# Performance work log

Measured on AMD Instinct MI355X. Metric: run time of the kernel, lower is better.

## Reference

```python
import jax, jax.numpy as jnp
import numpy as np

N_HEAD = 16


def setup_inputs() -> dict:
    key = jax.random.key(0)
    ks = jax.random.split(key, 9)
    d = 1024
    s = 0.02
    return {
        "x": jax.random.normal(ks[0], (8, 448, d), jnp.float32),
        "xa": jax.random.normal(ks[1], (8, 1500, d), jnp.float32),
        "Wq": jax.random.normal(ks[2], (d, d), jnp.float32) * s,
        "bq": jax.random.normal(ks[3], (d,), jnp.float32) * s,
        "Wk": jax.random.normal(ks[4], (d, d), jnp.float32) * s,
        "Wv": jax.random.normal(ks[5], (d, d), jnp.float32) * s,
        "bv": jax.random.normal(ks[6], (d,), jnp.float32) * s,
        "Wo": jax.random.normal(ks[7], (d, d), jnp.float32) * s,
        "bo": jax.random.normal(ks[8], (d,), jnp.float32) * s,
    }


def reference(x, xa, Wq, bq, Wk, Wv, bv, Wo, bo):
    B, T, D = x.shape
    S = xa.shape[1]
    H = N_HEAD
    Dh = D // H
    scale = Dh ** -0.25  # applied to both q and k, as in the original

    q = x @ Wq + bq            # [B,T,D]
    k = xa @ Wk                # [B,S,D] (no bias)
    v = xa @ Wv + bv           # [B,S,D]

    q = q.reshape(B, T, H, Dh) * scale
    k = k.reshape(B, S, H, Dh) * scale
    v = v.reshape(B, S, H, Dh)

    qk = jnp.einsum("bthd,bshd->bhts", q, k).astype(jnp.float32)  # pre-softmax logits
    w = jax.nn.softmax(qk, axis=-1).astype(q.dtype)
    wv = jnp.einsum("bhts,bshd->bthd", w, v).reshape(B, T, D)

    out = wv @ Wo + bo
    return out, qk
```

## Files before the change

### kernel.cpp

```cpp
#include <hip/hip_runtime.h>
#include <hip/hip_bf16.h>
#include <cstdint>
#include <cstddef>

typedef __bf16  bf16x8  __attribute__((ext_vector_type(8)));
typedef float   f32x4   __attribute__((ext_vector_type(4)));
typedef ushort  ushort8 __attribute__((ext_vector_type(8)));

#define ASYNC16(gp, lp)                                                        \
  __builtin_amdgcn_global_load_lds(                                            \
      (const __attribute__((address_space(1))) void*)(gp),                     \
      (__attribute__((address_space(3))) void*)(lp), 16, 0, 0)

__device__ __forceinline__ ushort f2bf(float f) {
  __hip_bfloat16 h = __float2bfloat16(f);
  ushort u; __builtin_memcpy(&u, &h, 2); return u;
}

#define SINF (-1e30f)

__global__ __launch_bounds__(256) void transpose_w(
    const float* __restrict__ W0, const float* __restrict__ W1,
    const float* __restrict__ W2, const float* __restrict__ W3,
    ushort* __restrict__ out) {
  __shared__ float tile[32][33];
  const float* W = blockIdx.z == 0 ? W0 : blockIdx.z == 1 ? W1
                 : blockIdx.z == 2 ? W2 : W3;
  ushort* T = out + (size_t)blockIdx.z * (1024u * 1024u);
  const int n0 = blockIdx.x * 32, k0 = blockIdx.y * 32;
  const int t = threadIdx.x;
  const int r = t >> 3, c = (t & 7) * 4;
  float4 v = *(const float4*)&W[(size_t)(k0 + r) * 1024 + n0 + c];
  tile[r][c + 0] = v.x; tile[r][c + 1] = v.y;
  tile[r][c + 2] = v.z; tile[r][c + 3] = v.w;
  __syncthreads();
  ushort4 o;
  o.x = f2bf(tile[c + 0][r]); o.y = f2bf(tile[c + 1][r]);
  o.z = f2bf(tile[c + 2][r]); o.w = f2bf(tile[c + 3][r]);
  *(ushort4*)&T[(size_t)(n0 + r) * 1024 + k0 + c] = o;
}

template <bool A_F32, bool C_F32>
__global__ __launch_bounds__(256) void gemm_bt(
    const void* __restrict__ Ap, const ushort* __restrict__ Bt,
    const float* __restrict__ bias, void* __restrict__ Cp,
    int M, float scale) {
  __shared__ ushort As[128 * 32];
  __shared__ ushort Bs[128 * 32];
  const int tid  = threadIdx.x;
  const int lane = tid & 63, w = tid >> 6;
  const int m15  = lane & 15, q4 = lane >> 4;
  const int wm   = w >> 1,  wn = w & 1;
  const int m0 = blockIdx.x * 128, n0 = blockIdx.y * 128;
  const int sr = lane >> 2;
  const int sc = (lane & 3) * 8;
  f32x4 acc[4][4] = {};
  for (int k0 = 0; k0 < 1024; k0 += 32) {
    __syncthreads();
    #pragma unroll
    for (int j = 0; j < 2; ++j) {
      int n = w * 2 + j;
      int r = n * 16 + sr;
      ASYNC16(&Bt[(size_t)(n0 + r) * 1024 + k0 + sc], &Bs[n * 512]);
    }
    if constexpr (A_F32) {
      const float* Af = (const float*)Ap;
      #pragma unroll
      for (int h = 0; h < 2; ++h) {
        int g = tid + h * 256;
        int row = g >> 2, kg = g & 3;
        int ga = min(m0 + row, M - 1);
        const float* src = &Af[(size_t)ga * 1024 + k0 + kg * 8];
        float4 a0 = *(const float4*)src;
        float4 a1 = *(const float4*)(src + 4);
        ushort8 u = { f2bf(a0.x), f2bf(a0.y), f2bf(a0.z), f2bf(a0.w),
                      f2bf(a1.x), f2bf(a1.y), f2bf(a1.z), f2bf(a1.w) };
        *(ushort8*)&As[row * 32 + kg * 8] = u;
      }
    } else {
      const ushort* Ab = (const ushort*)Ap;
      #pragma unroll
      for (int j = 0; j < 2; ++j) {
        int n = w * 2 + j;
        int r = n * 16 + sr;
        int ga = min(m0 + r, M - 1);
        ASYNC16(&Ab[(size_t)ga * 1024 + k0 + sc], &As[n * 512]);
      }
    }
    __syncthreads();
    bf16x8 af[4], bfr[4];
    #pragma unroll
    for (int i = 0; i < 4; ++i)
      af[i] = *(const bf16x8*)&As[(wm * 64 + i * 16 + m15) * 32 + q4 * 8];
    #pragma unroll
    for (int i = 0; i < 4; ++i)
      bfr[i] = *(const bf16x8*)&Bs[(wn * 64 + i * 16 + m15) * 32 + q4 * 8];
    #pragma unroll
    for (int i = 0; i < 4; ++i)
      #pragma unroll
      for (int j = 0; j < 4; ++j)
        acc[i][j] = __builtin_amdgcn_mfma_f32_16x16x32_bf16(af[i], bfr[j],
                                                            acc[i][j], 0, 0, 0);
  }
  #pragma unroll
  for (int j = 0; j < 4; ++j) {
    int col = n0 + wn * 64 + j * 16 + m15;
    float bb = bias ? bias[col] : 0.f;
    #pragma unroll
    for (int i = 0; i < 4; ++i) {
      #pragma unroll
      for (int r = 0; r < 4; ++r) {
        int row = m0 + wm * 64 + i * 16 + q4 * 4 + r;
        if (row < M) {
          float v = (acc[i][j][r] + bb) * scale;
          if constexpr (C_F32)
            ((float*)Cp)[(size_t)row * 1024 + col] = v;
          else
            ((ushort*)Cp)[(size_t)row * 1024 + col] = f2bf(v);
        }
      }
    }
  }
}

__global__ __launch_bounds__(256) void attn(
    const ushort* __restrict__ q_s, const ushort* __restrict__ k_s,
    const ushort* __restrict__ v_s, float* __restrict__ qk_out,
    ushort* __restrict__ wv) {
  __shared__ ushort Kb[64 * 64];
  __shared__ ushort Vt[64 * 72];
  __shared__ ushort Pw[4][16 * 72];
  const int tid  = threadIdx.x;
  const int lane = tid & 63, w = tid >> 6;
  const int m15  = lane & 15, q4 = lane >> 4;
  const int h = blockIdx.y, b = blockIdx.z;
  const int t0 = blockIdx.x * 64;
  const int trow = t0 + w * 16;
  const ushort* qrow = &q_s[(size_t)(b * 448 + trow + m15) * 1024 + h * 64];
  bf16x8 qf0 = *(const bf16x8*)&qrow[q4 * 8];
  bf16x8 qf1 = *(const bf16x8*)&qrow[32 + q4 * 8];
  f32x4 o[4] = {};
  float m_r[4] = {SINF, SINF, SINF, SINF};
  float l_r[4] = {0.f, 0.f, 0.f, 0.f};
  const int vr = tid >> 2;
  const int vc = (tid & 3) * 16;
  const int krb = lane >> 3;
  const int kc  = (lane & 7) * 8;
  for (int s0 = 0; s0 < 1500; s0 += 64) {
    __syncthreads();
    #pragma unroll
    for (int j = 0; j < 2; ++j) {
      int n = w * 2 + j;
      int sg = min(s0 + n * 8 + krb, 1499);
      ASYNC16(&k_s[(size_t)(b * 1500 + sg) * 1024 + h * 64 + kc], &Kb[n * 512]);
    }
    {
      int sg = min(s0 + vr, 1499);
      const ushort* vp = &v_s[(size_t)(b * 1500 + sg) * 1024 + h * 64 + vc];
      __align__(16) ushort vbuf[16];
      *(uint4*)&vbuf[0] = *(const uint4*)&vp[0];
      *(uint4*)&vbuf[8] = *(const uint4*)&vp[8];
      #pragma unroll
      for (int j = 0; j < 16; ++j) Vt[(vc + j) * 72 + vr] = vbuf[j];
    }
    __syncthreads();
    f32x4 lg[4];
    #pragma unroll
    for (int scol = 0; scol < 4; ++scol) {
      f32x4 a = {};
      bf16x8 kf0 = *(const bf16x8*)&Kb[(scol * 16 + m15) * 64 + q4 * 8];
      bf16x8 kf1 = *(const bf16x8*)&Kb[(scol * 16 + m15) * 64 + 32 + q4 * 8];
      a = __builtin_amdgcn_mfma_f32_16x16x32_bf16(qf0, kf0, a, 0, 0, 0);
      a = __builtin_amdgcn_mfma_f32_16x16x32_bf16(qf1, kf1, a, 0, 0, 0);
      lg[scol] = a;
    }
    float mc[4] = {SINF, SINF, SINF, SINF};
    #pragma unroll
    for (int scol = 0; scol < 4; ++scol) {
      bool valid = (s0 + scol * 16 + m15) < 1500;
      #pragma unroll
      for (int r = 0; r < 4; ++r)
        mc[r] = fmaxf(mc[r], valid ? lg[scol][r] : SINF);
    }
    #pragma unroll
    for (int off = 1; off < 16; off <<= 1)
      #pragma unroll
      for (int r = 0; r < 4; ++r)
        mc[r] = fmaxf(mc[r], __shfl_xor(mc[r], off));
    #pragma unroll
    for (int r = 0; r < 4; ++r) {
      float mn = fmaxf(m_r[r], mc[r]);
      float alpha = __expf(m_r[r] - mn);
      l_r[r] *= alpha;
      #pragma unroll
      for (int d = 0; d < 4; ++d) o[d][r] *= alpha;
      m_r[r] = mn;
    }
    float psum[4] = {0.f, 0.f, 0.f, 0.f};
    #pragma unroll
    for (int scol = 0; scol < 4; ++scol) {
      int sg = s0 + scol * 16 + m15;
      bool valid = sg < 1500;
      #pragma unroll
      for (int r = 0; r < 4; ++r) {
        float lv = lg[scol][r];
        float p = valid ? __expf(lv - m_r[r]) : 0.f;
        psum[r] += p;
        Pw[w][(q4 * 4 + r) * 72 + scol * 16 + m15] = f2bf(p);
        if (valid)
          qk_out[(size_t)((b * 16 + h) * 448 + trow + q4 * 4 + r) * 1500 + sg]
              = lv;
      }
    }
    #pragma unroll
    for (int off = 1; off < 16; off <<= 1)
      #pragma unroll
      for (int r = 0; r < 4; ++r)
        psum[r] += __shfl_xor(psum[r], off);
    #pragma unroll
    for (int r = 0; r < 4; ++r) l_r[r] += psum[r];
    #pragma unroll
    for (int ks = 0; ks < 2; ++ks) {
      bf16x8 pf = *(const bf16x8*)&Pw[w][m15 * 72 + ks * 32 + q4 * 8];
      #pragma unroll
      for (int d = 0; d < 4; ++d) {
        bf16x8 vf = *(const bf16x8*)&Vt[(d * 16 + m15) * 72 + ks * 32 + q4 * 8];
        o[d] = __builtin_amdgcn_mfma_f32_16x16x32_bf16(pf, vf, o[d], 0, 0, 0);
      }
    }
  }
  #pragma unroll
  for (int d = 0; d < 4; ++d)
    #pragma unroll
    for (int r = 0; r < 4; ++r) {
      float val = o[d][r] / l_r[r];
      wv[(size_t)(b * 448 + trow + q4 * 4 + r) * 1024 + h * 64 + d * 16 + m15]
          = f2bf(val);
    }
}

extern "C" void kernel_launch(void* const* d_in, const int* in_sizes, int n_in,
                              void* d_out, int out_size, void* d_ws,
                              size_t ws_size, hipStream_t stream) {
  const float* x  = (const float*)d_in[0];
  const float* xa = (const float*)d_in[1];
  const float* Wq = (const float*)d_in[2];
  const float* bq = (const float*)d_in[3];
  const float* Wk = (const float*)d_in[4];
  const float* Wv = (const float*)d_in[5];
  const float* bv = (const float*)d_in[6];
  const float* Wo = (const float*)d_in[7];
  const float* bo = (const float*)d_in[8];
  float* out = (float*)d_out;
  float* qk  = out + (size_t)8 * 448 * 1024;
  char* ws = (char*)d_ws;
  ushort* Wt   = (ushort*)ws;
  ushort* q_s  = (ushort*)(ws + (size_t)8  * 1024 * 1024);
  ushort* k_s  = (ushort*)(ws + (size_t)16 * 1024 * 1024);
  ushort* v_s  = (ushort*)(ws + (size_t)42 * 1024 * 1024);
  ushort* wv_s = (ushort*)(ws + (size_t)68 * 1024 * 1024);

  transpose_w<<<dim3(32, 32, 4), 256, 0, stream>>>(Wq, Wk, Wv, Wo, Wt);
  const float sc = 0.35355339059327373f;
  gemm_bt<true,  false><<<dim3(28, 8), 256, 0, stream>>>(x,  Wt,                bq,      q_s, 3584,  sc);
  gemm_bt<true,  false><<<dim3(94, 8), 256, 0, stream>>>(xa, Wt + 1u*1048576u,  nullptr, k_s, 12000, sc);
  gemm_bt<true,  false><<<dim3(94, 8), 256, 0, stream>>>(xa, Wt + 2u*1048576u,  bv,      v_s, 12000, 1.0f);
  attn<<<dim3(7, 16, 8), 256, 0, stream>>>(q_s, k_s, v_s, qk, wv_s);
  gemm_bt<false, true ><<<dim3(28, 8), 256, 0, stream>>>(wv_s, Wt + 3u*1048576u, bo,     out, 3584,  1.0f);
}
```

Baseline: 719.9 us.

## Pre-convert inputs to bf16, pre-transpose V, swizzle K tile in LDS

```diff
diff --git a/kernel.cpp b/kernel.cpp
--- a/kernel.cpp
+++ b/kernel.cpp
@@ -18,6 +18,19 @@
 }
 
 #define SINF (-1e30f)
+
+__global__ __launch_bounds__(256) void to_bf16(
+    const float* __restrict__ src, ushort* __restrict__ dst, int n8) {
+  int i = blockIdx.x * 256 + threadIdx.x;
+  const int stride = gridDim.x * 256;
+  for (; i < n8; i += stride) {
+    const float4* s = (const float4*)(src + (size_t)i * 8);
+    float4 a0 = s[0], a1 = s[1];
+    ushort8 u = { f2bf(a0.x), f2bf(a0.y), f2bf(a0.z), f2bf(a0.w),
+                  f2bf(a1.x), f2bf(a1.y), f2bf(a1.z), f2bf(a1.w) };
+    *(ushort8*)&dst[(size_t)i * 8] = u;
+  }
+}
 
 __global__ __launch_bounds__(256) void transpose_w(
     const float* __restrict__ W0, const float* __restrict__ W1,
@@ -40,6 +53,28 @@
   *(ushort4*)&T[(size_t)(n0 + r) * 1024 + k0 + c] = o;
 }
 
+__global__ __launch_bounds__(256) void transpose_v(
+    const ushort* __restrict__ v_s, ushort* __restrict__ v_t) {
+  __shared__ ushort tile[32][36];
+  const int bh = blockIdx.z;
+  const int b = bh >> 4, h = bh & 15;
+  const int d0 = blockIdx.y * 32;
+  const int s0 = blockIdx.x * 32;
+  const int t = threadIdx.x;
+  const int r = t >> 3, c4 = (t & 7) * 4;
+  const int s = s0 + r;
+  ushort4 v = {0, 0, 0, 0};
+  if (s < 1500)
+    v = *(const ushort4*)&v_s[(size_t)(b * 1500 + s) * 1024 + h * 64 + d0 + c4];
+  tile[r][c4 + 0] = v.x; tile[r][c4 + 1] = v.y;
+  tile[r][c4 + 2] = v.z; tile[r][c4 + 3] = v.w;
+  __syncthreads();
+  ushort4 o;
+  o.x = tile[c4 + 0][r]; o.y = tile[c4 + 1][r];
+  o.z = tile[c4 + 2][r]; o.w = tile[c4 + 3][r];
+  *(ushort4*)&v_t[((size_t)bh * 64 + d0 + r) * 1536 + s0 + c4] = o;
+}
+
 template <bool A_F32, bool C_F32>
 __global__ __launch_bounds__(256) void gemm_bt(
     const void* __restrict__ Ap, const ushort* __restrict__ Bt,
@@ -125,10 +160,9 @@
 
 __global__ __launch_bounds__(256) void attn(
     const ushort* __restrict__ q_s, const ushort* __restrict__ k_s,
-    const ushort* __restrict__ v_s, float* __restrict__ qk_out,
+    const ushort* __restrict__ v_t, float* __restrict__ qk_out,
     ushort* __restrict__ wv) {
   __shared__ ushort Kb[64 * 64];
-  __shared__ ushort Vt[64 * 72];
   __shared__ ushort Pw[4][16 * 72];
   const int tid  = threadIdx.x;
   const int lane = tid & 63, w = tid >> 6;
@@ -142,34 +176,28 @@
   f32x4 o[4] = {};
   float m_r[4] = {SINF, SINF, SINF, SINF};
   float l_r[4] = {0.f, 0.f, 0.f, 0.f};
-  const int vr = tid >> 2;
-  const int vc = (tid & 3) * 16;
   const int krb = lane >> 3;
-  const int kc  = (lane & 7) * 8;
+  const int kc_sw = (((lane & 7) ^ krb) * 8);
+  const ushort* vbase =
+      &v_t[((size_t)(b * 16 + h) * 64 + m15) * 1536 + q4 * 8];
   for (int s0 = 0; s0 < 1500; s0 += 64) {
     __syncthreads();
     #pragma unroll
     for (int j = 0; j < 2; ++j) {
       int n = w * 2 + j;
       int sg = min(s0 + n * 8 + krb, 1499);
-      ASYNC16(&k_s[(size_t)(b * 1500 + sg) * 1024 + h * 64 + kc], &Kb[n * 512]);
-    }
-    {
-      int sg = min(s0 + vr, 1499);
-      const ushort* vp = &v_s[(size_t)(b * 1500 + sg) * 1024 + h * 64 + vc];
-      __align__(16) ushort vbuf[16];
-      *(uint4*)&vbuf[0] = *(const uint4*)&vp[0];
-      *(uint4*)&vbuf[8] = *(const uint4*)&vp[8];
-      #pragma unroll
-      for (int j = 0; j < 16; ++j) Vt[(vc + j) * 72 + vr] = vbuf[j];
+      ASYNC16(&k_s[(size_t)(b * 1500 + sg) * 1024 + h * 64 + kc_sw],
+              &Kb[n * 512]);
     }
     __syncthreads();
     f32x4 lg[4];
     #pragma unroll
     for (int scol = 0; scol < 4; ++scol) {
+      const int r = scol * 16 + m15;
+      const int sw = (m15 & 7) * 8;
+      bf16x8 kf0 = *(const bf16x8*)&Kb[r * 64 + ((q4 * 8) ^ sw)];
+      bf16x8 kf1 = *(const bf16x8*)&Kb[r * 64 + ((32 + q4 * 8) ^ sw)];
       f32x4 a = {};
-      bf16x8 kf0 = *(const bf16x8*)&Kb[(scol * 16 + m15) * 64 + q4 * 8];
-      bf16x8 kf1 = *(const bf16x8*)&Kb[(scol * 16 + m15) * 64 + 32 + q4 * 8];
       a = __builtin_amdgcn_mfma_f32_16x16x32_bf16(qf0, kf0, a, 0, 0, 0);
       a = __builtin_amdgcn_mfma_f32_16x16x32_bf16(qf1, kf1, a, 0, 0, 0);
       lg[scol] = a;
@@ -221,12 +249,14 @@
     for (int r = 0; r < 4; ++r) l_r[r] += psum[r];
     #pragma unroll
     for (int ks = 0; ks < 2; ++ks) {
+      bf16x8 vf[4];
+      #pragma unroll
+      for (int d = 0; d < 4; ++d)
+        vf[d] = *(const bf16x8*)&vbase[(size_t)(d * 16) * 1536 + s0 + ks * 32];
       bf16x8 pf = *(const bf16x8*)&Pw[w][m15 * 72 + ks * 32 + q4 * 8];
       #pragma unroll
-      for (int d = 0; d < 4; ++d) {
-        bf16x8 vf = *(const bf16x8*)&Vt[(d * 16 + m15) * 72 + ks * 32 + q4 * 8];
-        o[d] = __builtin_amdgcn_mfma_f32_16x16x32_bf16(pf, vf, o[d], 0, 0, 0);
-      }
+      for (int d = 0; d < 4; ++d)
+        o[d] = __builtin_amdgcn_mfma_f32_16x16x32_bf16(pf, vf[d], o[d], 0, 0, 0);
     }
   }
   #pragma unroll
@@ -254,17 +284,23 @@
   float* out = (float*)d_out;
   float* qk  = out + (size_t)8 * 448 * 1024;
   char* ws = (char*)d_ws;
-  ushort* Wt   = (ushort*)ws;
-  ushort* q_s  = (ushort*)(ws + (size_t)8  * 1024 * 1024);
-  ushort* k_s  = (ushort*)(ws + (size_t)16 * 1024 * 1024);
-  ushort* v_s  = (ushort*)(ws + (size_t)42 * 1024 * 1024);
-  ushort* wv_s = (ushort*)(ws + (size_t)68 * 1024 * 1024);
-
+  ushort* Wt    = (ushort*)ws;
+  ushort* q_s   = (ushort*)(ws + (size_t)8   * 1024 * 1024);
+  ushort* k_s   = (ushort*)(ws + (size_t)16  * 1024 * 1024);
+  ushort* v_s   = (ushort*)(ws + (size_t)42  * 1024 * 1024);
+  ushort* wv_s  = (ushort*)(ws + (size_t)68  * 1024 * 1024);
+  ushort* x_bf  = (ushort*)(ws + (size_t)76  * 1024 * 1024);
+  ushort* xa_bf = (ushort*)(ws + (size_t)84  * 1024 * 1024);
+  ushort* v_t   = (ushort*)(ws + (size_t)112 * 1024 * 1024);
+
+  to_bf16<<<dim3(1792), 256, 0, stream>>>(x,  x_bf,  458752);
+  to_bf16<<<dim3(2048), 256, 0, stream>>>(xa, xa_bf, 1536000);
   transpose_w<<<dim3(32, 32, 4), 256, 0, stream>>>(Wq, Wk, Wv, Wo, Wt);
   const float sc = 0.35355339059327373f;
-  gemm_bt<true,  false><<<dim3(28, 8), 256, 0, stream>>>(x,  Wt,                bq,      q_s, 3584,  sc);
-  gemm_bt<true,  false><<<dim3(94, 8), 256, 0, stream>>>(xa, Wt + 1u*1048576u,  nullptr, k_s, 12000, sc);
-  gemm_bt<true,  false><<<dim3(94, 8), 256, 0, stream>>>(xa, Wt + 2u*1048576u,  bv,      v_s, 12000, 1.0f);
-  attn<<<dim3(7, 16, 8), 256, 0, stream>>>(q_s, k_s, v_s, qk, wv_s);
-  gemm_bt<false, true ><<<dim3(28, 8), 256, 0, stream>>>(wv_s, Wt + 3u*1048576u, bo,     out, 3584,  1.0f);
-}
+  gemm_bt<false, false><<<dim3(28, 8), 256, 0, stream>>>(x_bf,  Wt,               bq,      q_s, 3584,  sc);
+  gemm_bt<false, false><<<dim3(94, 8), 256, 0, stream>>>(xa_bf, Wt + 1u*1048576u, nullptr, k_s, 12000, sc);
+  gemm_bt<false, false><<<dim3(94, 8), 256, 0, stream>>>(xa_bf, Wt + 2u*1048576u, bv,      v_s, 12000, 1.0f);
+  transpose_v<<<dim3(48, 2, 128), 256, 0, stream>>>(v_s, v_t);
+  attn<<<dim3(7, 16, 8), 256, 0, stream>>>(q_s, k_s, v_t, qk, wv_s);
+  gemm_bt<false, true ><<<dim3(28, 8), 256, 0, stream>>>(wv_s, Wt + 3u*1048576u, bo,      out, 3584,  1.0f);
+}
```

After: 737.6 us. +2.5%, slower.
